# Kernel tuning notes

Hardware: AMD Instinct MI355X
Metric: run time of the kernel (lower is better)

## Reference

```python
import jax, jax.numpy as jnp
import numpy as np

N, M, G, H, ND, E = 4096, 8192, 8, 128, 16, 131072
MAX_PERIOD = 10000.0


def setup_inputs() -> dict:
    key = jax.random.key(0)
    ks = jax.random.split(key, 24)
    s = 0.05
    inp = {
        "x": jax.random.normal(ks[0], (N, ND), jnp.float32),
        "edge_index": jax.random.randint(ks[1], (2, E), 0, N),
        "timestep": jax.random.randint(ks[2], (G,), 0, 1000),
        "batch_map": jnp.sort(jax.random.randint(ks[3], (N,), 0, G)),
        "obj_nucleotide_mask": jax.random.randint(ks[4], (M,), 0, 3),
        "obj_central_mask": jax.random.bernoulli(ks[5], 0.3, (M,)),
        "obj_backbone_mask": jax.random.bernoulli(ks[6], 0.5, (M,)),
        "obj_x": jax.random.normal(ks[7], (M, ND - 3), jnp.float32),
        "obj_pos": jax.random.normal(ks[8], (M, 3), jnp.float32),
        "obj_batch": jnp.sort(jax.random.randint(ks[9], (M,), 0, G)),
        # params (stored [in, out]; y = x @ W + b)
        "W_node": s * jax.random.normal(ks[10], (ND, H)),
        "b_node": jnp.zeros((H,)),
        "W_cond": s * jax.random.normal(ks[11], (H, H)),
        "b_cond": jnp.zeros((H,)),
        "W_time": s * jax.random.normal(ks[12], (H, H)),
        "b_time": jnp.zeros((H,)),
        "W_conv1": s * jax.random.normal(ks[13], (H, H)),
        "b_conv1": jnp.zeros((H,)),
        "W_conv2": s * jax.random.normal(ks[14], (H, H)),
        "b_conv2": jnp.zeros((H,)),
        "W_out": s * jax.random.normal(ks[15], (H, ND)),
        "b_out": jnp.zeros((ND,)),
        "w_edge": s * jax.random.normal(ks[16], (2 * H,)),
        "b_edge": jnp.zeros(()),
    }
    return inp


def timestep_embedding(t, dim):
    half = dim // 2
    freqs = jnp.exp(-np.log(MAX_PERIOD) * jnp.arange(half, dtype=jnp.float32) / half)
    args = t[:, None].astype(jnp.float32) * freqs[None]
    return jnp.concatenate([jnp.cos(args), jnp.sin(args)], axis=-1)


def gcn_conv(xh, src, dst, norm, W, b, n):
    # x' = D^-1/2 (A+I) D^-1/2 (X W) + b  (PyG GCNConv, self-loops included in src/dst/norm)
    xw = xh @ W
    msg = xw[src] * norm[:, None]
    return jax.ops.segment_sum(msg, dst, num_segments=n) + b


def reference(x, edge_index, timestep, batch_map, obj_nucleotide_mask,
              obj_central_mask, obj_backbone_mask, obj_x, obj_pos, obj_batch,
              W_node, b_node, W_cond, b_cond, W_time, b_time,
              W_conv1, b_conv1, W_conv2, b_conv2, W_out, b_out, w_edge, b_edge):
    n = x.shape[0]
    # timestep embedding + projections
    time_emb = timestep_embedding(timestep, H)            # [G, H]
    node_emb = x @ W_node + b_node                        # [N, H]

    # condition node pooling (masked mean per graph)
    is_left = obj_nucleotide_mask == 0
    is_central = obj_central_mask
    is_right = obj_nucleotide_mask == 2
    is_base = ~obj_backbone_mask
    is_cond = is_left | (is_central & is_base) | (is_right & is_base)  # [M]
    cond_x = jnp.concatenate([obj_x, obj_pos], axis=1)    # [M, ND]
    cond_emb = cond_x @ W_node + b_node                   # [M, H]
    cm = is_cond.astype(cond_emb.dtype)
    sums = jax.ops.segment_sum(cond_emb * cm[:, None], obj_batch, num_segments=G)
    cnt = jax.ops.segment_sum(cm, obj_batch, num_segments=G)
    pooled = sums / jnp.maximum(cnt, 1.0)[:, None]        # [G, H]

    time_h = time_emb @ W_time + b_time                   # [G, H]
    cond_h = pooled @ W_cond + b_cond                     # [G, H]
    node_emb = node_emb + time_h[batch_map] + cond_h[batch_map]

    # GCN normalization with self-loops (shared by both conv layers)
    loop = jnp.arange(n)
    src = jnp.concatenate([edge_index[0], loop])
    dst = jnp.concatenate([edge_index[1], loop])
    deg = jax.ops.segment_sum(jnp.ones_like(src, jnp.float32), dst, num_segments=n)
    dinv = jnp.where(deg > 0, jax.lax.rsqrt(jnp.maximum(deg, 1.0)), 0.0)
    norm = dinv[src] * dinv[dst]

    h = jax.nn.relu(gcn_conv(node_emb, src, dst, norm, W_conv1, b_conv1, n))
    h = jax.nn.relu(gcn_conv(h, src, dst, norm, W_conv2, b_conv2, n))

    node_noise_pred = h @ W_out + b_out                   # [N, ND]

    # all-pairs edge logits: cat([h[row], h[col]]) @ w_edge + b
    # == (h @ w_left)[row] + (h @ w_right)[col] + b  (same math, avoids [P, 2H])
    row, col = jnp.triu_indices(n, k=1)
    s_l = h @ w_edge[:H]
    s_r = h @ w_edge[H:]
    edge_logits = s_l[row] + s_r[col] + b_edge            # [N*(N-1)/2]
    return (node_noise_pred, edge_logits)
```

## Files before the change

### kernel.cpp

```cpp
#include <hip/hip_runtime.h>

#define NN 4096
#define MM 8192
#define GG 8
#define HH 128
#define NDD 16
#define EE 131072
#define ZBLK 4
#define CBLK 64
#define COBJ (MM / CBLK)
#define WBLK 8
#define SB2 32
#define CAP 96

typedef float nt_f4 __attribute__((ext_vector_type(4)));

__global__ __launch_bounds__(256) void k_front(
    const float* __restrict__ obj_x, const float* __restrict__ obj_pos,
    const int* __restrict__ nuc, const int* __restrict__ central,
    const int* __restrict__ backbone, const int* __restrict__ obj_batch,
    int* __restrict__ cnt, float* __restrict__ partial, float* __restrict__ pcnt,
    const float* __restrict__ Wn, const float* __restrict__ Wc1,
    float* __restrict__ W1p) {
    int b = blockIdx.x, t = threadIdx.x;
    if (b < ZBLK) {
        ((int4*)cnt)[b * 256 + t] = make_int4(0, 0, 0, 0);
        return;
    }
    if (b < ZBLK + CBLK) {
        int cb = b - ZBLK;
        __shared__ float ls[GG * NDD];
        __shared__ float lc[GG];
        if (t < GG * NDD) ls[t] = 0.f;
        if (t < GG) lc[t] = 0.f;
        __syncthreads();
        int d = t & 15, oi = t >> 4;
        int base = cb * COBJ;
#pragma unroll
        for (int pass = 0; pass < COBJ / 16; pass++) {
            int o = base + pass * 16 + oi;
            int nv = nuc[o];
            bool isb = (backbone[o] == 0);
            bool cond = (nv == 0) || ((central[o] != 0) && isb) || ((nv == 2) && isb);
            if (cond) {
                float v = (d < 13) ? obj_x[o * 13 + d] : obj_pos[o * 3 + (d - 13)];
                int g = obj_batch[o];
                atomicAdd(&ls[g * NDD + d], v);
                if (d == 0) atomicAdd(&lc[g], 1.f);
            }
        }
        __syncthreads();
        if (t < GG * NDD) partial[cb * (GG * NDD) + t] = ls[t];
        if (t < GG) pcnt[cb * GG + t] = lc[t];
        return;
    }
    int wb = b - (ZBLK + CBLK);
    int j = t & 127, a = wb * 2 + (t >> 7);
    float acc = 0.f;
    for (int k = 0; k < HH; k++) acc += Wn[a * HH + k] * Wc1[k * HH + j];
    W1p[a * HH + j] = acc;
}

__global__ __launch_bounds__(1024) void k_mid(
    const int* __restrict__ e_src, const int* __restrict__ e_dst,
    int* __restrict__ cnt, int* __restrict__ col_idx,
    const int* __restrict__ timestep, const float* __restrict__ partial,
    const float* __restrict__ pcnt, const float* __restrict__ Wn,
    const float* __restrict__ bn, const float* __restrict__ Wt,
    const float* __restrict__ bt, const float* __restrict__ Wc,
    const float* __restrict__ bc, const float* __restrict__ Wc1,
    const float* __restrict__ x, const float* __restrict__ W1p,
    const int* __restrict__ bm, float* __restrict__ xw) {
    int b = blockIdx.x, t = threadIdx.x;
    if (b < SB2) {
        int i4 = b * 1024 + t;
        int4 d4 = ((const int4*)e_dst)[i4];
        int4 s4 = ((const int4*)e_src)[i4];
        int q;
        q = atomicAdd(&cnt[d4.x], 1); if (q < CAP) col_idx[d4.x * CAP + q] = s4.x;
        q = atomicAdd(&cnt[d4.y], 1); if (q < CAP) col_idx[d4.y * CAP + q] = s4.y;
        q = atomicAdd(&cnt[d4.z], 1); if (q < CAP) col_idx[d4.z * CAP + q] = s4.z;
        q = atomicAdd(&cnt[d4.w], 1); if (q < CAP) col_idx[d4.w * CAP + q] = s4.w;
        return;
    }
    int rb = b - SB2;
    int g = t >> 7, j = t & 127;
    __shared__ float s16[GG * NDD];
    __shared__ float cinv[GG];
    __shared__ float te[GG * HH];
    __shared__ float pool[GG * HH];
    __shared__ float v2[GG * HH];
    __shared__ float c1s[GG * HH];
    __shared__ float xt[32 * NDD];
    {
        float tv = (float)timestep[g];
        float val;
        if (j < 64) {
            float f = expf(-logf(10000.f) * (float)j / 64.f);
            val = cosf(tv * f);
        } else {
            float f = expf(-logf(10000.f) * (float)(j - 64) / 64.f);
            val = sinf(tv * f);
        }
        te[t] = val;
    }
    if (t < GG * NDD) {
        float s = 0.f;
        for (int q = 0; q < CBLK; q++) s += partial[q * (GG * NDD) + t];
        s16[t] = s;
    } else if (t < GG * NDD + GG) {
        int gg = t - GG * NDD;
        float c = 0.f;
        for (int q = 0; q < CBLK; q++) c += pcnt[q * GG + gg];
        cinv[gg] = 1.f / fmaxf(c, 1.f);
    }
    if (t >= 512) xt[t - 512] = x[rb * 32 * NDD + (t - 512)];
    __syncthreads();
    {
        float p = bn[j];
        float ci = cinv[g];
#pragma unroll
        for (int d = 0; d < NDD; d++) p += s16[g * NDD + d] * ci * Wn[d * HH + j];
        pool[t] = p;
    }
    __syncthreads();
    {
        float acc = bt[j] + bc[j] + bn[j];
#pragma unroll 4
        for (int k = 0; k < HH; k++)
            acc += te[g * HH + k] * Wt[k * HH + j] + pool[g * HH + k] * Wc[k * HH + j];
        v2[t] = acc;
    }
    __syncthreads();
    {
        float cc = 0.f;
#pragma unroll 4
        for (int k = 0; k < HH; k++) cc += v2[g * HH + k] * Wc1[k * HH + j];
        c1s[t] = cc;
    }
    __syncthreads();
    {
        int col = j, rh = g;
        int r0 = rb * 32;
        float acc[4] = {0.f, 0.f, 0.f, 0.f};
#pragma unroll
        for (int k = 0; k < NDD; k++) {
            float wv = W1p[k * HH + col];
#pragma unroll
            for (int i = 0; i < 4; i++) acc[i] += xt[(rh * 4 + i) * NDD + k] * wv;
        }
#pragma unroll
        for (int i = 0; i < 4; i++) {
            int row = r0 + rh * 4 + i;
            xw[row * HH + col] = acc[i] + c1s[bm[row] * HH + col];
        }
    }
}

__global__ __launch_bounds__(256, 8) void k_conv1(
    const float* __restrict__ xw, const int* __restrict__ cnt,
    const int* __restrict__ col_idx, const float* __restrict__ b1,
    const float* __restrict__ Wc2, float* __restrict__ xw2) {
    int t = threadIdx.x;
    int w = t >> 6, l = t & 63;
    int d = w >> 1, half = w & 1;
    int dst = blockIdx.x * 2 + d;
    int deg = cnt[dst];
    float dd = rsqrtf((float)deg + 1.f);
    int end = deg < CAP ? deg : CAP;
    int mid = end >> 1;
    const float2* xwp = (const float2*)xw;
    const int* ci = col_idx + dst * CAP;
    float2 acc = {0.f, 0.f};
    if (half == 0) {
        float2 sv = xwp[dst * 64 + l];
        acc.x = dd * sv.x;
        acc.y = dd * sv.y;
    }
    int e = half ? mid : 0;
    int e1 = half ? end : mid;
    for (; e + 3 < e1; e += 4) {
        int s0 = ci[e], s1 = ci[e + 1], s2 = ci[e + 2], s3 = ci[e + 3];
        float r0 = rsqrtf((float)cnt[s0] + 1.f), r1 = rsqrtf((float)cnt[s1] + 1.f);
        float r2 = rsqrtf((float)cnt[s2] + 1.f), r3 = rsqrtf((float)cnt[s3] + 1.f);
        float2 v0 = xwp[s0 * 64 + l], v1 = xwp[s1 * 64 + l];
        float2 v2 = xwp[s2 * 64 + l], v3 = xwp[s3 * 64 + l];
        acc.x += (r0 * v0.x + r1 * v1.x) + (r2 * v2.x + r3 * v3.x);
        acc.y += (r0 * v0.y + r1 * v1.y) + (r2 * v2.y + r3 * v3.y);
    }
    for (; e < e1; e++) {
        int s = ci[e];
        float r = rsqrtf((float)cnt[s] + 1.f);
        float2 v = xwp[s * 64 + l];
        acc.x += r * v.x;
        acc.y += r * v.y;
    }
    __shared__ float hr[2][HH];
    __shared__ float2 part[2][64];
    __shared__ float wsm[32 * HH];
    if (half == 1) part[d][l] = acc;
    __syncthreads();
    if (half == 0) {
        float2 pv = part[d][l];
        acc.x += pv.x;
        acc.y += pv.y;
        float2 h;
        h.x = fmaxf(dd * acc.x + b1[2 * l], 0.f);
        h.y = fmaxf(dd * acc.y + b1[2 * l + 1], 0.f);
        *(float2*)&hr[d][2 * l] = h;
    }
    float2 o = {0.f, 0.f};
#pragma unroll
    for (int q = 0; q < 4; q++) {
        __syncthreads();
        const float4* s4 = (const float4*)(Wc2 + q * 32 * HH);
        float4* d4 = (float4*)wsm;
#pragma unroll
        for (int i = 0; i < 4; i++) d4[i * 256 + t] = s4[i * 256 + t];
        __syncthreads();
#pragma unroll 4
        for (int k = 0; k < 16; k++) {
            int kk = half * 16 + k;
            float hk = hr[d][q * 32 + kk];
            float2 wv = *(const float2*)&wsm[kk * HH + 2 * l];
            o.x += hk * wv.x;
            o.y += hk * wv.y;
        }
    }
    __syncthreads();
    if (half == 1) part[d][l] = o;
    __syncthreads();
    if (half == 0) {
        float2 pv = part[d][l];
        o.x = (o.x + pv.x) * dd;
        o.y = (o.y + pv.y) * dd;
        ((float2*)xw2)[dst * 64 + l] = o;
    }
}

__global__ __launch_bounds__(256, 8) void k_conv2_head(
    const float* __restrict__ xw, const int* __restrict__ cnt,
    const int* __restrict__ col_idx, const float* __restrict__ b2,
    const float* __restrict__ Wo, const float* __restrict__ bo,
    const float* __restrict__ we, float* __restrict__ out_pred,
    float* __restrict__ sl, float* __restrict__ sr) {
    int t = threadIdx.x;
    int w = t >> 6, l = t & 63;
    int d = w >> 1, half = w & 1;
    int dst = blockIdx.x * 2 + d;
    int deg = cnt[dst];
    float dd = rsqrtf((float)deg + 1.f);
    int end = deg < CAP ? deg : CAP;
    int mid = end >> 1;
    const float2* xwp = (const float2*)xw;
    const int* ci = col_idx + dst * CAP;
    float2 acc = {0.f, 0.f};
    if (half == 0) acc = xwp[dst * 64 + l];
    int e = half ? mid : 0;
    int e1 = half ? end : mid;
    for (; e + 3 < e1; e += 4) {
        int s0 = ci[e], s1 = ci[e + 1], s2 = ci[e + 2], s3 = ci[e + 3];
        float2 v0 = xwp[s0 * 64 + l], v1 = xwp[s1 * 64 + l];
        float2 v2 = xwp[s2 * 64 + l], v3 = xwp[s3 * 64 + l];
        acc.x += (v0.x + v1.x) + (v2.x + v3.x);
        acc.y += (v0.y + v1.y) + (v2.y + v3.y);
    }
    for (; e < e1; e++) {
        float2 v = xwp[ci[e] * 64 + l];
        acc.x += v.x;
        acc.y += v.y;
    }
    __shared__ float hr[2][HH];
    __shared__ float2 part[2][64];
    if (half == 1) part[d][l] = acc;
    __syncthreads();
    if (half == 0) {
        float2 pv = part[d][l];
        acc.x += pv.x;
        acc.y += pv.y;
        float2 h;
        h.x = fmaxf(dd * acc.x + b2[2 * l], 0.f);
        h.y = fmaxf(dd * acc.y + b2[2 * l + 1], 0.f);
        *(float2*)&hr[d][2 * l] = h;
    }
    __syncthreads();
    if (half == 0) {
        int c = l & 15, pp = l >> 4;
        float a = 0.f;
#pragma unroll 4
        for (int k = pp * 32; k < pp * 32 + 32; k++) a += hr[d][k] * Wo[k * NDD + c];
        a += __shfl_xor(a, 16);
        a += __shfl_xor(a, 32);
        if (pp == 0) out_pred[dst * NDD + c] = a + bo[c];
    } else {
        float h0 = hr[d][l], h1v = hr[d][64 + l];
        float pl = h0 * we[l] + h1v * we[64 + l];
        float pr = h0 * we[HH + l] + h1v * we[HH + 64 + l];
        for (int off = 32; off; off >>= 1) {
            pl += __shfl_down(pl, off);
            pr += __shfl_down(pr, off);
        }
        if (l == 0) {
            sl[dst] = pl;
            sr[dst] = pr;
        }
    }
}

__global__ __launch_bounds__(256) void k_edges(const float* __restrict__ sl,
                                               const float* __restrict__ sr,
                                               const float* __restrict__ be_p,
                                               float* __restrict__ out) {
    int b = blockIdx.x, t = threadIdx.x;
    float be = be_p[0];
#pragma unroll
    for (int half = 0; half < 2; half++) {
        int r = half == 0 ? b : (NN - 2 - b);
        int off = r * (2 * NN - r - 1) / 2;
        int len = NN - 1 - r;
        float s = sl[r] + be;
        const float* sp = sr + r + 1;
        float* op = out + off;
        int hd = (4 - (off & 3)) & 3;
        if (hd > len) hd = len;
        if (t < hd) __builtin_nontemporal_store(s + sp[t], op + t);
        int body = (len - hd) >> 2;
        float* opb = op + hd;
        const float* spb = sp + hd;
        for (int i = t; i < body; i += 256) {
            int base = 4 * i;
            nt_f4 v;
            v.x = s + spb[base];
            v.y = s + spb[base + 1];
            v.z = s + spb[base + 2];
            v.w = s + spb[base + 3];
            __builtin_nontemporal_store(v, (nt_f4*)(opb + base));
        }
        int tail = hd + body * 4;
        int rem = len - tail;
        if (t < rem) __builtin_nontemporal_store(s + sp[tail + t], op + tail + t);
    }
}

extern "C" void kernel_launch(void* const* d_in, const int* in_sizes, int n_in,
                              void* d_out, int out_size, void* d_ws, size_t ws_size,
                              hipStream_t stream) {
    const float* x = (const float*)d_in[0];
    const int* e_src = (const int*)d_in[1];
    const int* e_dst = e_src + EE;
    const int* timestep = (const int*)d_in[2];
    const int* batch_map = (const int*)d_in[3];
    const int* nuc = (const int*)d_in[4];
    const int* central = (const int*)d_in[5];
    const int* backbone = (const int*)d_in[6];
    const float* obj_x = (const float*)d_in[7];
    const float* obj_pos = (const float*)d_in[8];
    const int* obj_batch = (const int*)d_in[9];
    const float* W_node = (const float*)d_in[10];
    const float* b_node = (const float*)d_in[11];
    const float* W_cond = (const float*)d_in[12];
    const float* b_cond = (const float*)d_in[13];
    const float* W_time = (const float*)d_in[14];
    const float* b_time = (const float*)d_in[15];
    const float* W_conv1 = (const float*)d_in[16];
    const float* b_conv1 = (const float*)d_in[17];
    const float* W_conv2 = (const float*)d_in[18];
    const float* b_conv2 = (const float*)d_in[19];
    const float* W_out = (const float*)d_in[20];
    const float* b_out = (const float*)d_in[21];
    const float* w_edge = (const float*)d_in[22];
    const float* b_edge = (const float*)d_in[23];

    float* ws = (float*)d_ws;
    float* bufA = ws;
    float* bufB = bufA + NN * HH;
    float* W1p = bufB + NN * HH;
    float* partial = W1p + NDD * HH;
    float* pcnt = partial + CBLK * GG * NDD;
    float* sl = pcnt + CBLK * GG;
    float* sr = sl + NN;
    int* cnt = (int*)(sr + NN);
    int* col_idx = cnt + NN;

    float* out_pred = (float*)d_out;
    float* out_edges = out_pred + NN * NDD;

    k_front<<<ZBLK + CBLK + WBLK, 256, 0, stream>>>(obj_x, obj_pos, nuc, central,
                                                    backbone, obj_batch, cnt, partial,
                                                    pcnt, W_node, W_conv1, W1p);
    k_mid<<<SB2 + NN / 32, 1024, 0, stream>>>(e_src, e_dst, cnt, col_idx, timestep,
                                              partial, pcnt, W_node, b_node, W_time,
                                              b_time, W_cond, b_cond, W_conv1, x,
                                              W1p, batch_map, bufA);
    k_conv1<<<NN / 2, 256, 0, stream>>>(bufA, cnt, col_idx, b_conv1, W_conv2, bufB);
    k_conv2_head<<<NN / 2, 256, 0, stream>>>(bufB, cnt, col_idx, b_conv2, W_out,
                                             b_out, w_edge, out_pred, sl, sr);
    k_edges<<<NN / 2, 256, 0, stream>>>(sl, sr, b_edge, out_edges);
}
```

Before: 172.8 us.

## Assign one wavefront per destination node in GCN conv kernels

```diff
diff --git a/kernel.cpp b/kernel.cpp
--- a/kernel.cpp
+++ b/kernel.cpp
@@ -56,9 +56,12 @@
     }
     int wb = b - (ZBLK + CBLK);
     int j = t & 127, a = wb * 2 + (t >> 7);
-    float acc = 0.f;
-    for (int k = 0; k < HH; k++) acc += Wn[a * HH + k] * Wc1[k * HH + j];
-    W1p[a * HH + j] = acc;
+    float a0 = 0.f, a1 = 0.f;
+    for (int k = 0; k < HH; k += 2) {
+        a0 += Wn[a * HH + k] * Wc1[k * HH + j];
+        a1 += Wn[a * HH + k + 1] * Wc1[(k + 1) * HH + j];
+    }
+    W1p[a * HH + j] = a0 + a1;
 }
 
 __global__ __launch_bounds__(1024) void k_mid(
@@ -125,18 +128,28 @@
     }
     __syncthreads();
     {
-        float acc = bt[j] + bc[j] + bn[j];
-#pragma unroll 4
-        for (int k = 0; k < HH; k++)
-            acc += te[g * HH + k] * Wt[k * HH + j] + pool[g * HH + k] * Wc[k * HH + j];
-        v2[t] = acc;
+        const float* teg = te + g * HH;
+        const float* poolg = pool + g * HH;
+        float a0 = 0.f, a1 = 0.f, a2 = 0.f, a3 = 0.f;
+        for (int k = 0; k < HH; k += 4) {
+            a0 += teg[k] * Wt[k * HH + j] + poolg[k] * Wc[k * HH + j];
+            a1 += teg[k + 1] * Wt[(k + 1) * HH + j] + poolg[k + 1] * Wc[(k + 1) * HH + j];
+            a2 += teg[k + 2] * Wt[(k + 2) * HH + j] + poolg[k + 2] * Wc[(k + 2) * HH + j];
+            a3 += teg[k + 3] * Wt[(k + 3) * HH + j] + poolg[k + 3] * Wc[(k + 3) * HH + j];
+        }
+        v2[t] = bt[j] + bc[j] + bn[j] + ((a0 + a1) + (a2 + a3));
     }
     __syncthreads();
     {
-        float cc = 0.f;
-#pragma unroll 4
-        for (int k = 0; k < HH; k++) cc += v2[g * HH + k] * Wc1[k * HH + j];
-        c1s[t] = cc;
+        const float* v2g = v2 + g * HH;
+        float a0 = 0.f, a1 = 0.f, a2 = 0.f, a3 = 0.f;
+        for (int k = 0; k < HH; k += 4) {
+            a0 += v2g[k] * Wc1[k * HH + j];
+            a1 += v2g[k + 1] * Wc1[(k + 1) * HH + j];
+            a2 += v2g[k + 2] * Wc1[(k + 2) * HH + j];
+            a3 += v2g[k + 3] * Wc1[(k + 3) * HH + j];
+        }
+        c1s[t] = (a0 + a1) + (a2 + a3);
     }
     __syncthreads();
     {
@@ -157,88 +170,82 @@
     }
 }
 
-__global__ __launch_bounds__(256, 8) void k_conv1(
+__global__ __launch_bounds__(512, 2) void k_conv1(
     const float* __restrict__ xw, const int* __restrict__ cnt,
     const int* __restrict__ col_idx, const float* __restrict__ b1,
     const float* __restrict__ Wc2, float* __restrict__ xw2) {
     int t = threadIdx.x;
     int w = t >> 6, l = t & 63;
-    int d = w >> 1, half = w & 1;
-    int dst = blockIdx.x * 2 + d;
+    int dst = blockIdx.x * 8 + w;
     int deg = cnt[dst];
     float dd = rsqrtf((float)deg + 1.f);
     int end = deg < CAP ? deg : CAP;
-    int mid = end >> 1;
     const float2* xwp = (const float2*)xw;
     const int* ci = col_idx + dst * CAP;
-    float2 acc = {0.f, 0.f};
-    if (half == 0) {
-        float2 sv = xwp[dst * 64 + l];
-        acc.x = dd * sv.x;
-        acc.y = dd * sv.y;
-    }
-    int e = half ? mid : 0;
-    int e1 = half ? end : mid;
-    for (; e + 3 < e1; e += 4) {
+    float2 sv = xwp[dst * 64 + l];
+    float2 acc;
+    acc.x = dd * sv.x;
+    acc.y = dd * sv.y;
+    int e = 0;
+    for (; e + 7 < end; e += 8) {
         int s0 = ci[e], s1 = ci[e + 1], s2 = ci[e + 2], s3 = ci[e + 3];
+        int s4 = ci[e + 4], s5 = ci[e + 5], s6 = ci[e + 6], s7 = ci[e + 7];
         float r0 = rsqrtf((float)cnt[s0] + 1.f), r1 = rsqrtf((float)cnt[s1] + 1.f);
         float r2 = rsqrtf((float)cnt[s2] + 1.f), r3 = rsqrtf((float)cnt[s3] + 1.f);
+        float r4 = rsqrtf((float)cnt[s4] + 1.f), r5 = rsqrtf((float)cnt[s5] + 1.f);
+        float r6 = rsqrtf((float)cnt[s6] + 1.f), r7 = rsqrtf((float)cnt[s7] + 1.f);
         float2 v0 = xwp[s0 * 64 + l], v1 = xwp[s1 * 64 + l];
         float2 v2 = xwp[s2 * 64 + l], v3 = xwp[s3 * 64 + l];
-        acc.x += (r0 * v0.x + r1 * v1.x) + (r2 * v2.x + r3 * v3.x);
-        acc.y += (r0 * v0.y + r1 * v1.y) + (r2 * v2.y + r3 * v3.y);
-    }
-    for (; e < e1; e++) {
+        float2 v4 = xwp[s4 * 64 + l], v5 = xwp[s5 * 64 + l];
+        float2 v6 = xwp[s6 * 64 + l], v7 = xwp[s7 * 64 + l];
+        acc.x += ((r0 * v0.x + r1 * v1.x) + (r2 * v2.x + r3 * v3.x)) +
+                 ((r4 * v4.x + r5 * v5.x) + (r6 * v6.x + r7 * v7.x));
+        acc.y += ((r0 * v0.y + r1 * v1.y) + (r2 * v2.y + r3 * v3.y)) +
+                 ((r4 * v4.y + r5 * v5.y) + (r6 * v6.y + r7 * v7.y));
+    }
+    for (; e < end; e++) {
         int s = ci[e];
         float r = rsqrtf((float)cnt[s] + 1.f);
         float2 v = xwp[s * 64 + l];
         acc.x += r * v.x;
         acc.y += r * v.y;
     }
-    __shared__ float hr[2][HH];
-    __shared__ float2 part[2][64];
+    __shared__ float hr[8][HH];
     __shared__ float wsm[32 * HH];
-    if (half == 1) part[d][l] = acc;
-    __syncthreads();
-    if (half == 0) {
-        float2 pv = part[d][l];
-        acc.x += pv.x;
-        acc.y += pv.y;
+    {
         float2 h;
         h.x = fmaxf(dd * acc.x + b1[2 * l], 0.f);
         h.y = fmaxf(dd * acc.y + b1[2 * l + 1], 0.f);
-        *(float2*)&hr[d][2 * l] = h;
-    }
-    float2 o = {0.f, 0.f};
+        *(float2*)&hr[w][2 * l] = h;
+    }
+    float ox0 = 0.f, ox1 = 0.f, oy0 = 0.f, oy1 = 0.f;
 #pragma unroll
     for (int q = 0; q < 4; q++) {
         __syncthreads();
-        const float4* s4 = (const float4*)(Wc2 + q * 32 * HH);
-        float4* d4 = (float4*)wsm;
-#pragma unroll
-        for (int i = 0; i < 4; i++) d4[i * 256 + t] = s4[i * 256 + t];
+        const float4* s4p = (const float4*)(Wc2 + q * 32 * HH);
+        float4* d4p = (float4*)wsm;
+#pragma unroll
+        for (int i = 0; i < 2; i++) d4p[i * 512 + t] = s4p[i * 512 + t];
         __syncthreads();
 #pragma unroll 4
         for (int k = 0; k < 16; k++) {
-            int kk = half * 16 + k;
-            float hk = hr[d][q * 32 + kk];
-            float2 wv = *(const float2*)&wsm[kk * HH + 2 * l];
-            o.x += hk * wv.x;
-            o.y += hk * wv.y;
-        }
-    }
-    __syncthreads();
-    if (half == 1) part[d][l] = o;
-    __syncthreads();
-    if (half == 0) {
-        float2 pv = part[d][l];
-        o.x = (o.x + pv.x) * dd;
-        o.y = (o.y + pv.y) * dd;
-        ((float2*)xw2)[dst * 64 + l] = o;
-    }
-}
-
-__global__ __launch_bounds__(256, 8) void k_conv2_head(
+            float h0 = hr[w][q * 32 + 2 * k];
+            float h1 = hr[w][q * 32 + 2 * k + 1];
+            float2 w0 = *(const float2*)&wsm[(2 * k) * HH + 2 * l];
+            float2 w1 = *(const float2*)&wsm[(2 * k + 1) * HH + 2 * l];
+            ox0 += h0 * w0.x;
+            oy0 += h0 * w0.y;
+            ox1 += h1 * w1.x;
+            oy1 += h1 * w1.y;
+        }
+    }
+    float2 o;
+    o.x = (ox0 + ox1) * dd;
+    o.y = (oy0 + oy1) * dd;
+    ((float2*)xw2)[dst * 64 + l] = o;
+}
+
+__global__ __launch_bounds__(256) void k_conv2_head(
     const float* __restrict__ xw, const int* __restrict__ cnt,
     const int* __restrict__ col_idx, const float* __restrict__ b2,
     const float* __restrict__ Wo, const float* __restrict__ bo,
@@ -246,54 +253,57 @@
     float* __restrict__ sl, float* __restrict__ sr) {
     int t = threadIdx.x;
     int w = t >> 6, l = t & 63;
-    int d = w >> 1, half = w & 1;
-    int dst = blockIdx.x * 2 + d;
+    int dst = blockIdx.x * 4 + w;
     int deg = cnt[dst];
     float dd = rsqrtf((float)deg + 1.f);
     int end = deg < CAP ? deg : CAP;
-    int mid = end >> 1;
     const float2* xwp = (const float2*)xw;
     const int* ci = col_idx + dst * CAP;
-    float2 acc = {0.f, 0.f};
-    if (half == 0) acc = xwp[dst * 64 + l];
-    int e = half ? mid : 0;
-    int e1 = half ? end : mid;
-    for (; e + 3 < e1; e += 4) {
+    float2 acc = xwp[dst * 64 + l];
+    int e = 0;
+    for (; e + 7 < end; e += 8) {
+        int s0 = ci[e], s1 = ci[e + 1], s2 = ci[e + 2], s3 = ci[e + 3];
+        int s4 = ci[e + 4], s5 = ci[e + 5], s6 = ci[e + 6], s7 = ci[e + 7];
+        float2 v0 = xwp[s0 * 64 + l], v1 = xwp[s1 * 64 + l];
+        float2 v2 = xwp[s2 * 64 + l], v3 = xwp[s3 * 64 + l];
+        float2 v4 = xwp[s4 * 64 + l], v5 = xwp[s5 * 64 + l];
+        float2 v6 = xwp[s6 * 64 + l], v7 = xwp[s7 * 64 + l];
+        acc.x += ((v0.x + v1.x) + (v2.x + v3.x)) + ((v4.x + v5.x) + (v6.x + v7.x));
+        acc.y += ((v0.y + v1.y) + (v2.y + v3.y)) + ((v4.y + v5.y) + (v6.y + v7.y));
+    }
+    for (; e + 3 < end; e += 4) {
         int s0 = ci[e], s1 = ci[e + 1], s2 = ci[e + 2], s3 = ci[e + 3];
         float2 v0 = xwp[s0 * 64 + l], v1 = xwp[s1 * 64 + l];
         float2 v2 = xwp[s2 * 64 + l], v3 = xwp[s3 * 64 + l];
         acc.x += (v0.x + v1.x) + (v2.x + v3.x);
         acc.y += (v0.y + v1.y) + (v2.y + v3.y);
     }
-    for (; e < e1; e++) {
+    for (; e < end; e++) {
         float2 v = xwp[ci[e] * 64 + l];
         acc.x += v.x;
         acc.y += v.y;
     }
-    __shared__ float hr[2][HH];
-    __shared__ float2 part[2][64];
-    if (half == 1) part[d][l] = acc;
+    float2 h;
+    h.x = fmaxf(dd * acc.x + b2[2 * l], 0.f);
+    h.y = fmaxf(dd * acc.y + b2[2 * l + 1], 0.f);
+    __shared__ float hr[4][HH];
+    *(float2*)&hr[w][2 * l] = h;
     __syncthreads();
-    if (half == 0) {
-        float2 pv = part[d][l];
-        acc.x += pv.x;
-        acc.y += pv.y;
-        float2 h;
-        h.x = fmaxf(dd * acc.x + b2[2 * l], 0.f);
-        h.y = fmaxf(dd * acc.y + b2[2 * l + 1], 0.f);
-        *(float2*)&hr[d][2 * l] = h;
-    }
-    __syncthreads();
-    if (half == 0) {
+    {
         int c = l & 15, pp = l >> 4;
-        float a = 0.f;
-#pragma unroll 4
-        for (int k = pp * 32; k < pp * 32 + 32; k++) a += hr[d][k] * Wo[k * NDD + c];
+        float a0 = 0.f, a1 = 0.f;
+#pragma unroll 8
+        for (int k = pp * 32; k < pp * 32 + 32; k += 2) {
+            a0 += hr[w][k] * Wo[k * NDD + c];
+            a1 += hr[w][k + 1] * Wo[(k + 1) * NDD + c];
+        }
+        float a = a0 + a1;
         a += __shfl_xor(a, 16);
         a += __shfl_xor(a, 32);
         if (pp == 0) out_pred[dst * NDD + c] = a + bo[c];
-    } else {
-        float h0 = hr[d][l], h1v = hr[d][64 + l];
+    }
+    {
+        float h0 = hr[w][l], h1v = hr[w][64 + l];
         float pl = h0 * we[l] + h1v * we[64 + l];
         float pr = h0 * we[HH + l] + h1v * we[HH + 64 + l];
         for (int off = 32; off; off >>= 1) {
@@ -392,8 +402,8 @@
                                               partial, pcnt, W_node, b_node, W_time,
                                               b_time, W_cond, b_cond, W_conv1, x,
                                               W1p, batch_map, bufA);
-    k_conv1<<<NN / 2, 256, 0, stream>>>(bufA, cnt, col_idx, b_conv1, W_conv2, bufB);
-    k_conv2_head<<<NN / 2, 256, 0, stream>>>(bufB, cnt, col_idx, b_conv2, W_out,
+    k_conv1<<<NN / 8, 512, 0, stream>>>(bufA, cnt, col_idx, b_conv1, W_conv2, bufB);
+    k_conv2_head<<<NN / 4, 256, 0, stream>>>(bufB, cnt, col_idx, b_conv2, W_out,
                                              b_out, w_edge, out_pred, sl, sr);
     k_edges<<<NN / 2, 256, 0, stream>>>(sl, sr, b_edge, out_edges);
 }
```

Result: no change. 169.9 us (-1.7%).
